# Optimization experiments

Measured on AMD Instinct MI355X. Metric: run time of the kernel, lower is better.

Reference implementation:

```python
import jax, jax.numpy as jnp
import numpy as np

N, K, D = 32768, 8192, 256


def setup_inputs() -> dict:
    key = jax.random.key(0)
    k1, k2 = jax.random.split(key)
    x = jax.random.normal(k1, (N, D), dtype=jnp.float32)
    vectors = jax.random.normal(k2, (K, D), dtype=jnp.float32)  # codebook
    return {"x": x, "vectors": vectors}


def reference(x, vectors):
    # torch.cdist(x[:,None,:], vectors[None]) followed by argmin over K.
    # Euclidean distance is monotone in squared distance, so argmin over the
    # without a sqrt, matching the original math exactly for the returned ids.
    x2 = jnp.sum(x * x, axis=-1, keepdims=True)          # [N, 1]
    c2 = jnp.sum(vectors * vectors, axis=-1)             # [K]
    d2 = x2 + c2 - 2.0 * jnp.matmul(x, vectors.T)        # [N, K]
    indices = jnp.argmin(d2, axis=-1)                    # [N]
    return indices.astype(jnp.int32)
```

## Files before the change

kernel.cpp:

```cpp
#include <hip/hip_runtime.h>
#include <stdint.h>
#include <stddef.h>


#define N_PTS 32768
#define K_CB  8192
#define D_DIM 256
#define TM 128
#define TN 128
#define SPLITK 4
#define KCHUNK (K_CB / SPLITK)
#define NTILES (KCHUNK / TN)
#define NCHUNKS (NTILES * 8)

#define WS_XH   0
#define WS_XL   (WS_XH + N_PTS * D_DIM * 2)
#define WS_CH   (WS_XL + N_PTS * D_DIM * 2)
#define WS_CL   (WS_CH + K_CB * D_DIM * 2)
#define WS_C2   (WS_CL + K_CB * D_DIM * 2)
#define WS_PD   (WS_C2 + K_CB * 4)
#define WS_PI   (WS_PD + SPLITK * N_PTS * 4)
#define WS_END  (WS_PI + SPLITK * N_PTS * 4)

typedef _Float16 half4v __attribute__((ext_vector_type(4)));
typedef _Float16 half8v __attribute__((ext_vector_type(8)));
typedef float    f32x4  __attribute__((ext_vector_type(4)));

__device__ __forceinline__ void gld16(const void* g, void* l) {
    __builtin_amdgcn_global_load_lds(
        (const __attribute__((address_space(1))) void*)g,
        (__attribute__((address_space(3))) void*)l, 16, 0, 0);
}


#define XBLOCKS (N_PTS * D_DIM / 4 / 256)
#define CBLOCKS (K_CB * D_DIM / 4 / 256)

__global__ void __launch_bounds__(256)
prep_kernel(const float* __restrict__ x, const float* __restrict__ vecs,
            _Float16* __restrict__ xh, _Float16* __restrict__ xl,
            _Float16* __restrict__ ch, _Float16* __restrict__ cl,
            float* __restrict__ c2) {
    const int b = blockIdx.x;
    if (b < XBLOCKS) {
        const int i = b * 256 + threadIdx.x;
        const float4 v = ((const float4*)x)[i];
        half4v h = {(_Float16)v.x, (_Float16)v.y, (_Float16)v.z, (_Float16)v.w};
        half4v l = {(_Float16)((v.x - (float)h[0]) * 2048.0f),
                    (_Float16)((v.y - (float)h[1]) * 2048.0f),
                    (_Float16)((v.z - (float)h[2]) * 2048.0f),
                    (_Float16)((v.w - (float)h[3]) * 2048.0f)};
        *(half4v*)(xh + (size_t)i * 4) = h;
        *(half4v*)(xl + (size_t)i * 4) = l;
    } else {
        const int i = (b - XBLOCKS) * 256 + threadIdx.x;
        const float4 v = ((const float4*)vecs)[i];
        half4v h = {(_Float16)v.x, (_Float16)v.y, (_Float16)v.z, (_Float16)v.w};
        half4v l = {(_Float16)((v.x - (float)h[0]) * 2048.0f),
                    (_Float16)((v.y - (float)h[1]) * 2048.0f),
                    (_Float16)((v.z - (float)h[2]) * 2048.0f),
                    (_Float16)((v.w - (float)h[3]) * 2048.0f)};
        *(half4v*)(ch + (size_t)i * 4) = h;
        *(half4v*)(cl + (size_t)i * 4) = l;
        float s = v.x * v.x + v.y * v.y + v.z * v.z + v.w * v.w;
#pragma unroll
        for (int off = 32; off > 0; off >>= 1) s += __shfl_down(s, off, 64);
        if ((threadIdx.x & 63) == 0) c2[i >> 6] = s;
    }
}

__global__ void __launch_bounds__(256)
cnorms_kernel(const float* __restrict__ vecs, float* __restrict__ c2) {
    int gwave = (blockIdx.x * 256 + threadIdx.x) >> 6;
    int lane  = threadIdx.x & 63;
    const float* src = vecs + (size_t)gwave * D_DIM;
    float4 v = ((const float4*)src)[lane];
    float s = v.x * v.x + v.y * v.y + v.z * v.z + v.w * v.w;
#pragma unroll
    for (int off = 32; off > 0; off >>= 1) s += __shfl_down(s, off, 64);
    if (lane == 0) c2[gwave] = s;
}


__global__ void __launch_bounds__(256, 2)
vq_main_fast(const _Float16* __restrict__ xh_g, const _Float16* __restrict__ xl_g,
             const _Float16* __restrict__ ch_g, const _Float16* __restrict__ cl_g,
             const float* __restrict__ c2, float* __restrict__ pd, int* __restrict__ pi) {
    __shared__ __align__(16) char lds[65536];

    const int t    = threadIdx.x;
    const int lane = t & 63;
    const int wv   = t >> 6;
    const int wy   = wv >> 1, wx = wv & 1;
    const int fr   = lane & 15;
    const int g    = lane >> 4;

    const int split = blockIdx.x & (SPLITK - 1);
    const int pbase = (blockIdx.x >> 2) * TM;
    const int kbase = split * KCHUNK;

    const int srowoff = (lane >> 2) * (D_DIM * 2)
                      + ((((lane & 3) ^ ((lane >> 3) & 3))) << 4);
    const char* xh_s = (const char*)xh_g + (size_t)(pbase + wv * 32) * (D_DIM * 2) + srowoff;
    const char* xl_s = (const char*)xl_g + (size_t)(pbase + wv * 32) * (D_DIM * 2) + srowoff;
    const char* ch_s = (const char*)ch_g + (size_t)(kbase + wv * 32) * (D_DIM * 2) + srowoff;
    const char* cl_s = (const char*)cl_g + (size_t)(kbase + wv * 32) * (D_DIM * 2) + srowoff;
    const int stA = wv * 32 * 64;

    const int skey = (fr >> 1) & 3;
    int aoff[4], boff[4];
#pragma unroll
    for (int i = 0; i < 4; ++i) {
        aoff[i] = (wy * 64 + i * 16 + fr) * 64 + ((g ^ skey) << 4);
        boff[i] = 16384 + (wx * 64 + i * 16 + fr) * 64 + ((g ^ skey) << 4);
    }

    f32x4 acc[4][4];

    auto STAGE = [&](char* L, int c) {
        const size_t kofs = (size_t)(c >> 3) * (TN * D_DIM * 2);
        const int gofs = (c & 7) * 64;
#pragma unroll
        for (int q = 0; q < 2; ++q) {
            gld16(xh_s + q * 8192 + gofs, L +         stA + q * 1024);
            gld16(xl_s + q * 8192 + gofs, L +  8192 + stA + q * 1024);
            gld16(ch_s + kofs + q * 8192 + gofs, L + 16384 + stA + q * 1024);
            gld16(cl_s + kofs + q * 8192 + gofs, L + 24576 + stA + q * 1024);
        }
    };

    auto COMPUTE = [&](const char* L) {
        half8v a1[4], a2[4], a3[4];
#pragma unroll
        for (int i = 0; i < 4; ++i) {
            const char* p = L + aoff[i];
            a1[i] = *(const half8v*)p;
            a3[i] = *(const half8v*)(p + 8192);
            a2[i] = a1[i] * (_Float16)4.8828125e-4f;
        }
#pragma unroll
        for (int j = 0; j < 4; ++j) {
            const char* p = L + boff[j];
            half8v b1 = *(const half8v*)p;
            half8v b2 = *(const half8v*)(p + 8192);
            half8v b3 = b1 * (_Float16)4.8828125e-4f;
#pragma unroll
            for (int i = 0; i < 4; ++i) {
                acc[i][j] = __builtin_amdgcn_mfma_f32_16x16x32_f16(a1[i], b1, acc[i][j], 0, 0, 0);
                acc[i][j] = __builtin_amdgcn_mfma_f32_16x16x32_f16(a2[i], b2, acc[i][j], 0, 0, 0);
                acc[i][j] = __builtin_amdgcn_mfma_f32_16x16x32_f16(a3[i], b3, acc[i][j], 0, 0, 0);
            }
        }
    };

    float best[16];
    int   bidx[16];
#pragma unroll
    for (int i = 0; i < 16; ++i) { best[i] = 3.4e38f; bidx[i] = 0; }

    STAGE(lds, 0);
    __syncthreads();

#pragma unroll 1
    for (int kt = 0; kt < NTILES; ++kt) {
#pragma unroll
        for (int i = 0; i < 4; ++i)
#pragma unroll
            for (int j = 0; j < 4; ++j) {
                f32x4 z = {0.f, 0.f, 0.f, 0.f};
                acc[i][j] = z;
            }

#pragma unroll 1
        for (int du = 0; du < 4; ++du) {
            const int c = kt * 8 + du * 2;
            if (c + 1 < NCHUNKS) STAGE(lds + 32768, c + 1);
            COMPUTE(lds);
            __syncthreads();
            if (c + 2 < NCHUNKS) STAGE(lds, c + 2);
            COMPUTE(lds + 32768);
            __syncthreads();
        }

        const int ktbase = kbase + kt * TN;
#pragma unroll
        for (int j = 0; j < 4; ++j) {
            const int cg = ktbase + wx * 64 + j * 16 + fr;
            const float c2v = c2[cg];
#pragma unroll
            for (int i = 0; i < 4; ++i)
#pragma unroll
                for (int r = 0; r < 4; ++r) {
                    const float v = fmaf(-2.0f, acc[i][j][r], c2v);
                    const int s = i * 4 + r;
                    if (v < best[s]) { best[s] = v; bidx[s] = cg; }
                }
        }
    }

    __syncthreads();
    float* rd = (float*)lds;
    int*   ri = (int*)lds + 256;
#pragma unroll
    for (int i = 0; i < 4; ++i)
#pragma unroll
        for (int r = 0; r < 4; ++r) {
            float bv = best[i * 4 + r];
            int   bi = bidx[i * 4 + r];
#pragma unroll
            for (int off = 1; off < 16; off <<= 1) {
                const float ov = __shfl_xor(bv, off, 64);
                const int   oi = __shfl_xor(bi, off, 64);
                if (ov < bv || (ov == bv && oi < bi)) { bv = ov; bi = oi; }
            }
            if (fr == 0) {
                const int rowl = wy * 64 + i * 16 + g * 4 + r;
                rd[rowl * 2 + wx] = bv;
                ri[rowl * 2 + wx] = bi;
            }
        }
    __syncthreads();
    if (t < TM) {
        float b0 = rd[t * 2];
        int   i0 = ri[t * 2];
        const float b1 = rd[t * 2 + 1];
        const int   i1 = ri[t * 2 + 1];
        if (b1 < b0 || (b1 == b0 && i1 < i0)) { b0 = b1; i0 = i1; }
        pd[split * N_PTS + pbase + t] = b0;
        pi[split * N_PTS + pbase + t] = i0;
    }
}


#define BK 32
#define LS (BK + 4)

__device__ inline half8v load8(const _Float16* p) {
    half4v a = *(const half4v*)p;
    half4v b = *(const half4v*)(p + 4);
    return __builtin_shufflevector(a, b, 0, 1, 2, 3, 4, 5, 6, 7);
}

struct Trip { _Float16 h, s2, l2; };

__device__ inline Trip cvt3(float v) {
    Trip t;
    _Float16 hh = (_Float16)v;
    float hf = (float)hh;
    t.h  = hh;
    t.s2 = (_Float16)(hf * 4.8828125e-4f);
    t.l2 = (_Float16)((v - hf) * 2048.0f);
    return t;
}

__global__ void __launch_bounds__(256, 2)
vq_main_v3(const float* __restrict__ x, const float* __restrict__ vecs,
           const float* __restrict__ c2, float* __restrict__ pd, int* __restrict__ pi) {
    __shared__ _Float16 lds[6 * TM * LS];
    _Float16* xh  = lds;
    _Float16* xs2 = lds + 1 * TM * LS;
    _Float16* xl2 = lds + 2 * TM * LS;
    _Float16* ch  = lds + 3 * TM * LS;
    _Float16* cl2 = lds + 4 * TM * LS;
    _Float16* cs2 = lds + 5 * TM * LS;

    const int t     = threadIdx.x;
    const int split = blockIdx.x & (SPLITK - 1);
    const int pbase = (blockIdx.x >> 2) * TM;
    const int kbase = split * KCHUNK;

    const int lane = t & 63;
    const int wv   = t >> 6;
    const int wy   = wv >> 1, wx = wv & 1;
    const int fr   = lane & 15;
    const int g    = lane >> 4;
    const int kb   = g * 8;

    const int srow = t >> 3;
    const int sc4  = (t & 7) * 4;

    float best[16];
    int   bidx[16];
#pragma unroll
    for (int i = 0; i < 16; ++i) { best[i] = 3.4e38f; bidx[i] = 0; }

    for (int kt = 0; kt < NTILES; ++kt) {
        const int ktbase = kbase + kt * TN;
        f32x4 acc[4][4];
#pragma unroll
        for (int i = 0; i < 4; ++i)
#pragma unroll
            for (int j = 0; j < 4; ++j) {
                f32x4 z = {0.f, 0.f, 0.f, 0.f};
                acc[i][j] = z;
            }
        for (int dk = 0; dk < D_DIM; dk += BK) {
            __syncthreads();
#pragma unroll
            for (int p = 0; p < 4; ++p) {
                const int row = srow + p * 32;
                const float4 v = *(const float4*)&x[(size_t)(pbase + row) * D_DIM + dk + sc4];
                const Trip t0 = cvt3(v.x), t1 = cvt3(v.y), t2 = cvt3(v.z), t3 = cvt3(v.w);
                half4v h  = {t0.h,  t1.h,  t2.h,  t3.h};
                half4v s2 = {t0.s2, t1.s2, t2.s2, t3.s2};
                half4v l2 = {t0.l2, t1.l2, t2.l2, t3.l2};
                *(half4v*)&xh [row * LS + sc4] = h;
                *(half4v*)&xs2[row * LS + sc4] = s2;
                *(half4v*)&xl2[row * LS + sc4] = l2;
                const float4 w = *(const float4*)&vecs[(size_t)(ktbase + row) * D_DIM + dk + sc4];
                const Trip u0 = cvt3(w.x), u1 = cvt3(w.y), u2 = cvt3(w.z), u3 = cvt3(w.w);
                half4v hc = {u0.h,  u1.h,  u2.h,  u3.h};
                half4v sc = {u0.s2, u1.s2, u2.s2, u3.s2};
                half4v lc = {u0.l2, u1.l2, u2.l2, u3.l2};
                *(half4v*)&ch [row * LS + sc4] = hc;
                *(half4v*)&cs2[row * LS + sc4] = sc;
                *(half4v*)&cl2[row * LS + sc4] = lc;
            }
            __syncthreads();
            half8v a1[4], a2[4], a3[4], b1[4], b2[4], b3[4];
#pragma unroll
            for (int i = 0; i < 4; ++i) {
                const int aoff = (wy * 64 + i * 16 + fr) * LS + kb;
                a1[i] = load8(&xh [aoff]);
                a2[i] = load8(&xs2[aoff]);
                a3[i] = load8(&xl2[aoff]);
                const int boff2 = (wx * 64 + i * 16 + fr) * LS + kb;
                b1[i] = load8(&ch [boff2]);
                b2[i] = load8(&cl2[boff2]);
                b3[i] = load8(&cs2[boff2]);
            }
#pragma unroll
            for (int i = 0; i < 4; ++i)
#pragma unroll
                for (int j = 0; j < 4; ++j) {
                    acc[i][j] = __builtin_amdgcn_mfma_f32_16x16x32_f16(a1[i], b1[j], acc[i][j], 0, 0, 0);
                    acc[i][j] = __builtin_amdgcn_mfma_f32_16x16x32_f16(a2[i], b2[j], acc[i][j], 0, 0, 0);
                    acc[i][j] = __builtin_amdgcn_mfma_f32_16x16x32_f16(a3[i], b3[j], acc[i][j], 0, 0, 0);
                }
        }
#pragma unroll
        for (int j = 0; j < 4; ++j) {
            const int cg = ktbase + wx * 64 + j * 16 + fr;
            const float c2v = c2[cg];
#pragma unroll
            for (int i = 0; i < 4; ++i)
#pragma unroll
                for (int r = 0; r < 4; ++r) {
                    const float v = fmaf(-2.0f, acc[i][j][r], c2v);
                    const int s = i * 4 + r;
                    if (v < best[s]) { best[s] = v; bidx[s] = cg; }
                }
        }
    }
    __syncthreads();
    float* rd = (float*)lds;
    int*   ri = (int*)lds + 256;
#pragma unroll
    for (int i = 0; i < 4; ++i)
#pragma unroll
        for (int r = 0; r < 4; ++r) {
            float bv = best[i * 4 + r];
            int   bi = bidx[i * 4 + r];
#pragma unroll
            for (int off = 1; off < 16; off <<= 1) {
                const float ov = __shfl_xor(bv, off, 64);
                const int   oi = __shfl_xor(bi, off, 64);
                if (ov < bv || (ov == bv && oi < bi)) { bv = ov; bi = oi; }
            }
            if (fr == 0) {
                const int rowl = wy * 64 + i * 16 + g * 4 + r;
                rd[rowl * 2 + wx] = bv;
                ri[rowl * 2 + wx] = bi;
            }
        }
    __syncthreads();
    if (t < TM) {
        float b0 = rd[t * 2];
        int   i0 = ri[t * 2];
        const float b1 = rd[t * 2 + 1];
        const int   i1 = ri[t * 2 + 1];
        if (b1 < b0 || (b1 == b0 && i1 < i0)) { b0 = b1; i0 = i1; }
        pd[split * N_PTS + pbase + t] = b0;
        pi[split * N_PTS + pbase + t] = i0;
    }
}


__global__ void __launch_bounds__(256)
vq_combine(const float* __restrict__ pd, const int* __restrict__ pi,
           int* __restrict__ out) {
    const int p = blockIdx.x * 256 + threadIdx.x;
    float bb = pd[p];
    int   bi = pi[p];
#pragma unroll
    for (int s = 1; s < SPLITK; ++s) {
        const float v  = pd[s * N_PTS + p];
        const int   vi = pi[s * N_PTS + p];
        if (v < bb || (v == bb && vi < bi)) { bb = v; bi = vi; }
    }
    out[p] = bi;
}

extern "C" void kernel_launch(void* const* d_in, const int* in_sizes, int n_in,
                              void* d_out, int out_size, void* d_ws, size_t ws_size,
                              hipStream_t stream) {
    const float* x    = (const float*)d_in[0];
    const float* vecs = (const float*)d_in[1];
    int* out = (int*)d_out;
    char* ws = (char*)d_ws;

    if (ws_size >= (size_t)WS_END) {
        _Float16* xh = (_Float16*)(ws + WS_XH);
        _Float16* xl = (_Float16*)(ws + WS_XL);
        _Float16* ch = (_Float16*)(ws + WS_CH);
        _Float16* cl = (_Float16*)(ws + WS_CL);
        float* c2 = (float*)(ws + WS_C2);
        float* pd = (float*)(ws + WS_PD);
        int*   pi = (int*)(ws + WS_PI);

        hipLaunchKernelGGL(prep_kernel, dim3(XBLOCKS + CBLOCKS), dim3(256), 0, stream,
                           x, vecs, xh, xl, ch, cl, c2);
        hipLaunchKernelGGL(vq_main_fast, dim3((N_PTS / TM) * SPLITK), dim3(256), 0, stream,
                           xh, xl, ch, cl, c2, pd, pi);
        hipLaunchKernelGGL(vq_combine, dim3(N_PTS / 256), dim3(256), 0, stream,
                           pd, pi, out);
    } else {
        float* c2 = (float*)ws;
        float* pd = (float*)ws + K_CB;
        int*   pi = (int*)((float*)ws + K_CB + SPLITK * N_PTS);
        hipLaunchKernelGGL(cnorms_kernel, dim3(K_CB / 4), dim3(256), 0, stream,
                           vecs, c2);
        hipLaunchKernelGGL(vq_main_v3, dim3((N_PTS / TM) * SPLITK), dim3(256), 0, stream,
                           x, vecs, c2, pd, pi);
        hipLaunchKernelGGL(vq_combine, dim3(N_PTS / 256), dim3(256), 0, stream,
                           pd, pi, out);
    }
}
```

Measured before the change: 501.4 us.

## Drop LDS double buffering to single buffer and raise occupancy to four blocks

Cuts the shared-memory buffer from two 32KB stages to one and raises the launch bound to allow four blocks per CU. Each chunk is now loaded, synchronized, and computed in sequence with two barriers. The aim is to hide latency through more resident waves instead of software prefetch. In exchange, overlap of global loads with MFMA work inside a block is lost, and the tighter register budget from the higher occupancy target may force spills of the large accumulator and best/index arrays.

```diff
diff --git a/kernel.cpp b/kernel.cpp
--- a/kernel.cpp
+++ b/kernel.cpp
@@ -82,11 +82,11 @@
 }
 
 
-__global__ void __launch_bounds__(256, 2)
+__global__ void __launch_bounds__(256, 4)
 vq_main_fast(const _Float16* __restrict__ xh_g, const _Float16* __restrict__ xl_g,
              const _Float16* __restrict__ ch_g, const _Float16* __restrict__ cl_g,
              const float* __restrict__ c2, float* __restrict__ pd, int* __restrict__ pi) {
-    __shared__ __align__(16) char lds[65536];
+    __shared__ __align__(16) char lds[32768];
 
     const int t    = threadIdx.x;
     const int lane = t & 63;
@@ -105,7 +105,7 @@
     const char* xl_s = (const char*)xl_g + (size_t)(pbase + wv * 32) * (D_DIM * 2) + srowoff;
     const char* ch_s = (const char*)ch_g + (size_t)(kbase + wv * 32) * (D_DIM * 2) + srowoff;
     const char* cl_s = (const char*)cl_g + (size_t)(kbase + wv * 32) * (D_DIM * 2) + srowoff;
-    const int stA = wv * 32 * 64;
+    const int stA = wv * 2048;
 
     const int skey = (fr >> 1) & 3;
     int aoff[4], boff[4];
@@ -117,30 +117,30 @@
 
     f32x4 acc[4][4];
 
-    auto STAGE = [&](char* L, int c) {
+    auto STAGE = [&](int c) {
         const size_t kofs = (size_t)(c >> 3) * (TN * D_DIM * 2);
         const int gofs = (c & 7) * 64;
 #pragma unroll
         for (int q = 0; q < 2; ++q) {
-            gld16(xh_s + q * 8192 + gofs, L +         stA + q * 1024);
-            gld16(xl_s + q * 8192 + gofs, L +  8192 + stA + q * 1024);
-            gld16(ch_s + kofs + q * 8192 + gofs, L + 16384 + stA + q * 1024);
-            gld16(cl_s + kofs + q * 8192 + gofs, L + 24576 + stA + q * 1024);
+            gld16(xh_s + q * 8192 + gofs, lds +         stA + q * 1024);
+            gld16(xl_s + q * 8192 + gofs, lds +  8192 + stA + q * 1024);
+            gld16(ch_s + kofs + q * 8192 + gofs, lds + 16384 + stA + q * 1024);
+            gld16(cl_s + kofs + q * 8192 + gofs, lds + 24576 + stA + q * 1024);
         }
     };
 
-    auto COMPUTE = [&](const char* L) {
+    auto COMPUTE = [&]() {
         half8v a1[4], a2[4], a3[4];
 #pragma unroll
         for (int i = 0; i < 4; ++i) {
-            const char* p = L + aoff[i];
+            const char* p = lds + aoff[i];
             a1[i] = *(const half8v*)p;
             a3[i] = *(const half8v*)(p + 8192);
             a2[i] = a1[i] * (_Float16)4.8828125e-4f;
         }
 #pragma unroll
         for (int j = 0; j < 4; ++j) {
-            const char* p = L + boff[j];
+            const char* p = lds + boff[j];
             half8v b1 = *(const half8v*)p;
             half8v b2 = *(const half8v*)(p + 8192);
             half8v b3 = b1 * (_Float16)4.8828125e-4f;
@@ -158,9 +158,6 @@
 #pragma unroll
     for (int i = 0; i < 16; ++i) { best[i] = 3.4e38f; bidx[i] = 0; }
 
-    STAGE(lds, 0);
-    __syncthreads();
-
 #pragma unroll 1
     for (int kt = 0; kt < NTILES; ++kt) {
 #pragma unroll
@@ -172,14 +169,12 @@
             }
 
 #pragma unroll 1
-        for (int du = 0; du < 4; ++du) {
-            const int c = kt * 8 + du * 2;
-            if (c + 1 < NCHUNKS) STAGE(lds + 32768, c + 1);
-            COMPUTE(lds);
+        for (int dkc = 0; dkc < 8; ++dkc) {
+            const int c = kt * 8 + dkc;
             __syncthreads();
-            if (c + 2 < NCHUNKS) STAGE(lds, c + 2);
-            COMPUTE(lds + 32768);
+            STAGE(c);
             __syncthreads();
+            COMPUTE();
         }
 
         const int ktbase = kbase + kt * TN;
```

New measurement: 616.1 us. 1.23x slower.
